# Kernel optimization log

Hardware: AMD Instinct MI355X
Metric: run time of the kernel (lower is better)

Reference implementation:

```python
import jax, jax.numpy as jnp
import numpy as np

# dims
T, B, IN, OUT = 100, 128, 512, 512
# LIF constants (match torch defaults / init_kwargs)
TAU_TRACE, TAU_MEM, TAU_SYN, DT = 20.0, 20.0, 5.0, 1.0
THRESH, SSB = 1.0, 0.03


def setup_inputs() -> dict:
    key = jax.random.key(0)
    k1, k2 = jax.random.split(key)
    input_spikes = (jax.random.uniform(k1, (T, B, IN)) < 0.1).astype(jnp.float32)
    W = jax.random.normal(k2, (OUT, IN), dtype=jnp.float32) * (1.0 / IN ** 0.5)
    return {"input_spikes": input_spikes, "W": W}


def reference(input_spikes, W):
    alpha = jnp.exp(jnp.asarray(-DT / TAU_SYN, jnp.float32))   # synaptic decay
    beta = jnp.exp(jnp.asarray(-DT / TAU_MEM, jnp.float32))    # membrane decay
    gamma = jnp.exp(jnp.asarray(-DT / TAU_TRACE, jnp.float32)) # trace decay
    Tn, Bn, _ = input_spikes.shape
    out_f, in_f = W.shape
    I0 = jnp.zeros((Bn, out_f), jnp.float32)
    U0 = jnp.zeros((Bn, out_f), jnp.float32)
    tr0 = jnp.zeros((Bn, out_f, in_f), jnp.float32)

    def step(carry, x_t):
        I, U, trace = carry
        I = alpha * I + x_t @ W.T                      # (B, out)
        U = beta * U + I
        S = (U >= THRESH).astype(jnp.float32)
        U_pre = U                                      # first U_hist append (pre-reset)
        U = U - S * THRESH                             # reset
        du = jnp.abs(U - THRESH)
        sigma_prime = 1.0 / (1.0 + SSB * du) ** 2      # SuperSpike surrogate
        # eligibility trace: outer product of surrogate grad and input spikes
        trace = gamma * trace + sigma_prime[:, :, None] * x_t[:, None, :]
        U_post = U                                     # second U_hist append (post-reset)
        U = U - S * THRESH                             # second subtraction (as in source)
        return (I, U, trace), (S, U_pre, U_post)

    (_, _, trace), (S, U_pre, U_post) = jax.lax.scan(step, (I0, U0, tr0), input_spikes)
    # interleave pre/post membrane snapshots -> (2T, B, out), matching the torch stack order
    U_hist = jnp.stack([U_pre, U_post], axis=1).reshape(2 * Tn, Bn, out_f)
    return S, U_hist, trace
```

## Files before the change

kernel.cpp:

```cpp
#include <hip/hip_runtime.h>

#define T_STEPS 100
#define B_N     128
#define IN_F    512
#define OUT_F   512
#define KPAD    128

#define ALPHA_D 0.8187307530779818
#define BETA_D  0.9512294245007140

typedef __attribute__((ext_vector_type(8))) short bf16x8;
typedef __attribute__((ext_vector_type(4))) float f32x4;

static __device__ __forceinline__ unsigned int f2bf(float f) {
    union { float f; unsigned int u; } v; v.f = f;
    return (v.u + 0x7FFFu + ((v.u >> 16) & 1u)) >> 16;
}

__global__ __launch_bounds__(256) void transposeW(const float* __restrict__ W,
                                                  float* __restrict__ Wt) {
    __shared__ float tile[32][33];
    const int bx = blockIdx.x & 15;
    const int by = blockIdx.x >> 4;
    const int tx = threadIdx.x & 31;
    const int ty = threadIdx.x >> 5;
#pragma unroll
    for (int k = 0; k < 32; k += 8) {
        int o = by * 32 + ty + k;
        tile[ty + k][tx] = W[o * IN_F + bx * 32 + tx];
    }
    __syncthreads();
#pragma unroll
    for (int k = 0; k < 32; k += 8) {
        int i = bx * 32 + ty + k;
        Wt[i * OUT_F + by * 32 + tx] = tile[tx][ty + k];
    }
}

__global__ __launch_bounds__(256) void syn_plus(const float* __restrict__ x,
                                                const float* __restrict__ Wt,
                                                double* __restrict__ C,
                                                unsigned short* __restrict__ Xbf,
                                                int nconv) {
    const int tid = threadIdx.x;

    if ((int)blockIdx.x < nconv) {
        const int cb = blockIdx.x;
        const int b  = cb & (B_N - 1);
        const int i0 = (cb >> 7) * 128;
#pragma unroll
        for (int r = 0; r < 8; ++r) {
            const int g = tid + r * 256;
            const int i = i0 + (g & 127);
            const int c = g >> 7;
            unsigned int h[4];
#pragma unroll
            for (int jj = 0; jj < 4; ++jj) {
                const int t0 = c * 8 + jj * 2, t1 = t0 + 1;
                float v0 = 0.f, v1 = 0.f;
                if (t0 < T_STEPS) v0 = x[(size_t)t0 * (B_N * IN_F) + b * IN_F + i];
                if (t1 < T_STEPS) v1 = x[(size_t)t1 * (B_N * IN_F) + b * IN_F + i];
                h[jj] = f2bf(v0) | (f2bf(v1) << 16);
            }
            *(uint4*)((char*)Xbf + (size_t)(b * IN_F + i) * (KPAD * 2) + c * 16) =
                make_uint4(h[0], h[1], h[2], h[3]);
        }
        return;
    }

    const int tb = (int)blockIdx.x - nconv;

    __shared__ int s_idx[IN_F];
    __shared__ int s_cnt;

    if (tid < 64) {
        const float* xr = x + (size_t)tb * IN_F;
        int base = 0;
#pragma unroll
        for (int j = 0; j < 8; ++j) {
            const float v = xr[j * 64 + tid];
            const unsigned long long m = __ballot(v > 0.5f);
            if (v > 0.5f) {
                const int pos = base + __popcll(m & ((1ull << tid) - 1ull));
                s_idx[pos] = j * 64 + tid;
            }
            base += __popcll(m);
        }
        if (tid == 0) s_cnt = base;
    }
    __syncthreads();

    const int cnt = s_cnt;
    double c0 = 0.0, c1 = 0.0;
    const float* W0 = Wt + tid;
    const float* W1 = Wt + tid + 256;
    for (int k = 0; k < cnt; ++k) {
        const int i = s_idx[k];
        c0 += (double)W0[(size_t)i * OUT_F];
        c1 += (double)W1[(size_t)i * OUT_F];
    }

    double* Cr = C + (size_t)tb * OUT_F;
    Cr[tid]       = c0;
    Cr[tid + 256] = c1;
}

#define LIF_STEP(BUF, J, CB)                                                   \
    {                                                                          \
        const int t = (CB) * 10 + (J);                                         \
        I = ALPHA_D * I + BUF[J];                                              \
        U = BETA_D * U + I;                                                    \
        const double Sv = (U >= 1.0) ? 1.0 : 0.0;                              \
        S_out[(size_t)t * N + pos] = (float)Sv;                                \
        Uh[(size_t)(2 * t) * N + pos] = (float)U;                              \
        U -= Sv;                                                               \
        Uh[(size_t)(2 * t + 1) * N + pos] = (float)U;                          \
        if (Pq) {                                                              \
            const float du = fabsf((float)U - 1.0f);                           \
            const float dd = 1.0f + 0.03f * du;                                \
            const float pv = __expf(-0.05f * (float)(T_STEPS - 1 - t)) / (dd * dd); \
            const unsigned int hw = f2bf(pv);                                  \
            if ((J) & 1) Pq[(size_t)pos * 64 + (t >> 1)] = plo | (hw << 16);   \
            else plo = hw;                                                     \
        }                                                                      \
        U -= Sv;                                                               \
    }

__global__ __launch_bounds__(256) void lif_pointwise(const double* __restrict__ C,
                                                     float* __restrict__ S_out,
                                                     float* __restrict__ Uh,
                                                     unsigned int* __restrict__ Pq) {
    const int pos = blockIdx.x * 256 + threadIdx.x;
    const size_t N = (size_t)B_N * OUT_F;

    double I = 0.0, U = 0.0;
    double bufA[10], bufB[10];
    unsigned int plo = 0;

#pragma unroll
    for (int j = 0; j < 10; ++j) bufA[j] = C[(size_t)j * N + pos];

    for (int cb = 0; cb < 10; cb += 2) {
#pragma unroll
        for (int j = 0; j < 10; ++j) bufB[j] = C[((size_t)(cb + 1) * 10 + j) * N + pos];
#pragma unroll
        for (int j = 0; j < 10; ++j) LIF_STEP(bufA, j, cb)
        if (cb + 2 < 10) {
#pragma unroll
            for (int j = 0; j < 10; ++j) bufA[j] = C[((size_t)(cb + 2) * 10 + j) * N + pos];
        }
#pragma unroll
        for (int j = 0; j < 10; ++j) LIF_STEP(bufB, j, cb + 1)
    }

    if (Pq) {
#pragma unroll
        for (int k = 0; k < 14; ++k) Pq[(size_t)pos * 64 + 50 + k] = 0u;
    }
}

__global__ __launch_bounds__(256) void trace_mfma2(const unsigned short* __restrict__ Pbf,
                                                   const unsigned short* __restrict__ Xbf,
                                                   float* __restrict__ trace) {
    __shared__ char smem[49152];
    char* const pbase = smem;
    char* const xbase = smem + 32768;

    const int idx  = blockIdx.x;
    const int xcd  = idx & 7;
    const int slot = idx >> 3;
    const int b    = xcd * 16 + (slot >> 5);
    const int tile = slot & 31;
    const int ot   = tile >> 3;
    const int it   = tile & 7;
    const int tid  = threadIdx.x;

    const char* const Pg = (const char*)Pbf + (size_t)(b * OUT_F + ot * 128) * (KPAD * 2);
    const char* const Xg = (const char*)Xbf + (size_t)(b * IN_F + it * 64) * (KPAD * 2);

#pragma unroll
    for (int r = 0; r < 8; ++r) {
        const int chunk = tid + r * 256;
        const int row   = chunk >> 4;
        const int c     = chunk & 15;
        const unsigned int loff = (unsigned int)(row * 256) +
            ((unsigned int)(c * 16) ^ ((unsigned int)(row & 7) << 4));
        *(uint4*)(pbase + loff) = *(const uint4*)(Pg + (size_t)row * 256 + c * 16);
    }
#pragma unroll
    for (int r = 0; r < 4; ++r) {
        const int chunk = tid + r * 256;
        const int row   = chunk >> 4;
        const int c     = chunk & 15;
        const unsigned int loff = (unsigned int)(row * 256) +
            ((unsigned int)(c * 16) ^ ((unsigned int)(row & 7) << 4));
        *(uint4*)(xbase + loff) = *(const uint4*)(Xg + (size_t)row * 256 + c * 16);
    }
    __syncthreads();

    const int w    = tid >> 6;
    const int l    = tid & 63;
    const int lo16 = l & 15;
    const int g4   = l >> 4;

    f32x4 acc[2][4];
#pragma unroll
    for (int m = 0; m < 2; ++m)
#pragma unroll
        for (int n = 0; n < 4; ++n) acc[m][n] = (f32x4){0.f, 0.f, 0.f, 0.f};

#pragma unroll
    for (int kk = 0; kk < 4; ++kk) {
        bf16x8 af[2], bfr[4];
#pragma unroll
        for (int m = 0; m < 2; ++m) {
            const int row = w * 32 + m * 16 + lo16;
            const unsigned int off = (unsigned int)(row * 256 + kk * 64 + g4 * 16)
                                     ^ ((unsigned int)(row & 7) << 4);
            af[m] = *(const bf16x8*)(pbase + off);
        }
#pragma unroll
        for (int n = 0; n < 4; ++n) {
            const int row = n * 16 + lo16;
            const unsigned int off = (unsigned int)(row * 256 + kk * 64 + g4 * 16)
                                     ^ ((unsigned int)(row & 7) << 4);
            bfr[n] = *(const bf16x8*)(xbase + off);
        }
#pragma unroll
        for (int m = 0; m < 2; ++m)
#pragma unroll
            for (int n = 0; n < 4; ++n)
                acc[m][n] = __builtin_amdgcn_mfma_f32_16x16x32_bf16(af[m], bfr[n], acc[m][n], 0, 0, 0);
    }

    __syncthreads();
    float* const obuf = (float*)smem;
#pragma unroll
    for (int m = 0; m < 2; ++m)
#pragma unroll
        for (int n = 0; n < 4; ++n)
#pragma unroll
            for (int rr = 0; rr < 4; ++rr)
                obuf[(w * 32 + m * 16 + g4 * 4 + rr) * 68 + n * 16 + lo16] = acc[m][n][rr];
    __syncthreads();

    float* const tb = trace + (size_t)b * (OUT_F * IN_F) + (size_t)(ot * 128) * IN_F + it * 64;
#pragma unroll
    for (int p = 0; p < 8; ++p) {
        const int row  = p * 16 + (tid >> 4);
        const int col4 = (tid & 15) * 4;
        const f32x4 v = *(const f32x4*)&obuf[row * 68 + col4];
        __builtin_nontemporal_store(v, (f32x4*)(tb + (size_t)row * IN_F + col4));
    }
}

__global__ __launch_bounds__(256) void trace_mfma(const float* __restrict__ x,
                                                  const float* __restrict__ Uh,
                                                  float* __restrict__ trace) {
    __shared__ unsigned short Pa[128 * 128];
    __shared__ unsigned short Xb[128 * 128];

    const int idx  = blockIdx.x;
    const int xcd  = idx & 7;
    const int slot = idx >> 3;
    const int b    = xcd * 16 + (slot >> 4);
    const int tile = slot & 15;
    const int ot   = tile >> 2;
    const int it   = tile & 3;
    const int tid  = threadIdx.x;

    char* const pbase = (char*)Pa;
    char* const xbase = (char*)Xb;

#pragma unroll
    for (int r = 0; r < 8; ++r) {
        const int g  = tid + r * 256;
        const int i  = g & 127;
        const int kg = g >> 7;
        unsigned int h[4];
#pragma unroll
        for (int jj = 0; jj < 4; ++jj) {
            const int t0 = kg * 8 + jj * 2, t1 = t0 + 1;
            float v0 = 0.f, v1 = 0.f;
            if (t0 < T_STEPS) v0 = x[(size_t)t0 * (B_N * IN_F) + b * IN_F + it * 128 + i];
            if (t1 < T_STEPS) v1 = x[(size_t)t1 * (B_N * IN_F) + b * IN_F + it * 128 + i];
            h[jj] = f2bf(v0) | (f2bf(v1) << 16);
        }
        unsigned int off = (unsigned int)(i * 256 + kg * 16) ^ ((unsigned int)(i & 7) << 4);
        *(uint4*)(xbase + off) = make_uint4(h[0], h[1], h[2], h[3]);
    }

#pragma unroll
    for (int r = 0; r < 8; ++r) {
        const int g  = tid + r * 256;
        const int o  = g & 127;
        const int kg = g >> 7;
        unsigned int h[4];
#pragma unroll
        for (int jj = 0; jj < 4; ++jj) {
            unsigned int hw[2];
#pragma unroll
            for (int e = 0; e < 2; ++e) {
                const int t = kg * 8 + jj * 2 + e;
                float p = 0.f;
                if (t < T_STEPS) {
                    const float u  = Uh[(size_t)(2 * t + 1) * (B_N * OUT_F) + b * OUT_F + ot * 128 + o];
                    const float du = fabsf(u - 1.0f);
                    const float d  = 1.0f + 0.03f * du;
                    const float gp = __expf(-0.05f * (float)(T_STEPS - 1 - t));
                    p = gp / (d * d);
                }
                hw[e] = f2bf(p);
            }
            h[jj] = hw[0] | (hw[1] << 16);
        }
        unsigned int off = (unsigned int)(o * 256 + kg * 16) ^ ((unsigned int)(o & 7) << 4);
        *(uint4*)(pbase + off) = make_uint4(h[0], h[1], h[2], h[3]);
    }
    __syncthreads();

    const int w    = tid >> 6;
    const int l    = tid & 63;
    const int wo   = (w >> 1) * 64;
    const int wi   = (w & 1) * 64;
    const int lo16 = l & 15;
    const int g4   = l >> 4;

    f32x4 acc[4][4];
#pragma unroll
    for (int m = 0; m < 4; ++m)
#pragma unroll
        for (int n = 0; n < 4; ++n) acc[m][n] = (f32x4){0.f, 0.f, 0.f, 0.f};

#pragma unroll
    for (int kk = 0; kk < 4; ++kk) {
        bf16x8 af[4], bfr[4];
#pragma unroll
        for (int m = 0; m < 4; ++m) {
            const int row = wo + m * 16 + lo16;
            const unsigned int off = (unsigned int)(row * 256 + kk * 64 + g4 * 16)
                                     ^ ((unsigned int)(row & 7) << 4);
            af[m] = *(const bf16x8*)(pbase + off);
        }
#pragma unroll
        for (int n = 0; n < 4; ++n) {
            const int row = wi + n * 16 + lo16;
            const unsigned int off = (unsigned int)(row * 256 + kk * 64 + g4 * 16)
                                     ^ ((unsigned int)(row & 7) << 4);
            bfr[n] = *(const bf16x8*)(xbase + off);
        }
#pragma unroll
        for (int m = 0; m < 4; ++m)
#pragma unroll
            for (int n = 0; n < 4; ++n)
                acc[m][n] = __builtin_amdgcn_mfma_f32_16x16x32_bf16(af[m], bfr[n], acc[m][n], 0, 0, 0);
    }

    float* tb = trace + (size_t)b * (OUT_F * IN_F);
#pragma unroll
    for (int m = 0; m < 4; ++m) {
#pragma unroll
        for (int rr = 0; rr < 4; ++rr) {
            const int o = ot * 128 + wo + m * 16 + g4 * 4 + rr;
#pragma unroll
            for (int n = 0; n < 4; ++n) {
                const int i = it * 128 + wi + n * 16 + lo16;
                tb[(size_t)o * IN_F + i] = acc[m][n][rr];
            }
        }
    }
}

extern "C" void kernel_launch(void* const* d_in, const int* in_sizes, int n_in,
                              void* d_out, int out_size, void* d_ws, size_t ws_size,
                              hipStream_t stream) {
    const float* x = (const float*)d_in[0];
    const float* W = (const float*)d_in[1];

    float* out   = (float*)d_out;
    float* S_out = out;
    float* Uh    = out + (size_t)T_STEPS * B_N * OUT_F;
    float* trace = Uh + (size_t)2 * T_STEPS * B_N * OUT_F;

    const size_t WT_BYTES = (size_t)IN_F * OUT_F * 4;
    const size_t BF_BYTES = (size_t)B_N * 512 * KPAD * 2;
    const bool   ws_ok    = ws_size >= WT_BYTES + 2 * BF_BYTES;

    float*          Wt  = (float*)d_ws;
    unsigned short* Xbf = (unsigned short*)((char*)d_ws + WT_BYTES);
    unsigned short* Pbf = (unsigned short*)((char*)d_ws + WT_BYTES + BF_BYTES);

    double* C = (double*)trace;

    const int nconv = ws_ok ? 512 : 0;

    transposeW<<<256, 256, 0, stream>>>(W, Wt);
    syn_plus<<<T_STEPS * B_N + nconv, 256, 0, stream>>>(x, Wt, C, Xbf, nconv);
    lif_pointwise<<<B_N * OUT_F / 256, 256, 0, stream>>>(C, S_out, Uh,
                                                         ws_ok ? (unsigned int*)Pbf : nullptr);
    if (ws_ok)
        trace_mfma2<<<32 * B_N, 256, 0, stream>>>(Pbf, Xbf, trace);
    else
        trace_mfma<<<16 * B_N, 256, 0, stream>>>(x, Uh, trace);
}
```

Before: 160.4 us.

## Make trace kernel persistent over input tiles with double-buffered X prefetch

The trace MFMA kernel now launches 512 blocks, each covering one (batch, 128-row output) slab. It keeps the P fragments in registers for the whole slab and loops over the 8 input tiles, prefetching the next X tile into a second LDS buffer while the current one is in use. Output is written straight from the accumulators as scalar nontemporal stores instead of being staged through LDS for 16-byte vector stores. This saves redundant P loads and launch overhead, but the scalar, strided stores may hurt write coalescing on a kernel dominated by the 134 MB trace write, and having fewer blocks lowers parallelism.

Result: slower. 173.3 us (+8.0%).

```diff
diff --git a/kernel.cpp b/kernel.cpp
--- a/kernel.cpp
+++ b/kernel.cpp
@@ -159,24 +159,23 @@
     }
 }
 
-__global__ __launch_bounds__(256) void trace_mfma2(const unsigned short* __restrict__ Pbf,
+__global__ __launch_bounds__(256) void trace_mfma3(const unsigned short* __restrict__ Pbf,
                                                    const unsigned short* __restrict__ Xbf,
                                                    float* __restrict__ trace) {
-    __shared__ char smem[49152];
-    char* const pbase = smem;
-    char* const xbase = smem + 32768;
-
-    const int idx  = blockIdx.x;
-    const int xcd  = idx & 7;
-    const int slot = idx >> 3;
-    const int b    = xcd * 16 + (slot >> 5);
-    const int tile = slot & 31;
-    const int ot   = tile >> 3;
-    const int it   = tile & 7;
-    const int tid  = threadIdx.x;
-
-    const char* const Pg = (const char*)Pbf + (size_t)(b * OUT_F + ot * 128) * (KPAD * 2);
-    const char* const Xg = (const char*)Xbf + (size_t)(b * IN_F + it * 64) * (KPAD * 2);
+    __shared__ char smem[65536];
+    char* const Pl = smem;
+    char* const X0 = smem + 32768;
+    char* const X1 = smem + 49152;
+
+    const int idx = blockIdx.x;
+    const int xcd = idx & 7;
+    const int s   = idx >> 3;
+    const int b   = xcd * 16 + (s >> 2);
+    const int ot  = s & 3;
+    const int tid = threadIdx.x;
+
+    const char* const Pg  = (const char*)Pbf + (size_t)(b * OUT_F + ot * 128) * 256;
+    const char* const Xgb = (const char*)Xbf + (size_t)b * IN_F * 256;
 
 #pragma unroll
     for (int r = 0; r < 8; ++r) {
@@ -185,7 +184,7 @@
         const int c     = chunk & 15;
         const unsigned int loff = (unsigned int)(row * 256) +
             ((unsigned int)(c * 16) ^ ((unsigned int)(row & 7) << 4));
-        *(uint4*)(pbase + loff) = *(const uint4*)(Pg + (size_t)row * 256 + c * 16);
+        *(uint4*)(Pl + loff) = *(const uint4*)(Pg + (size_t)row * 256 + c * 16);
     }
 #pragma unroll
     for (int r = 0; r < 4; ++r) {
@@ -194,7 +193,7 @@
         const int c     = chunk & 15;
         const unsigned int loff = (unsigned int)(row * 256) +
             ((unsigned int)(c * 16) ^ ((unsigned int)(row & 7) << 4));
-        *(uint4*)(xbase + loff) = *(const uint4*)(Xg + (size_t)row * 256 + c * 16);
+        *(uint4*)(X0 + loff) = *(const uint4*)(Xgb + (size_t)row * 256 + c * 16);
     }
     __syncthreads();
 
@@ -203,54 +202,80 @@
     const int lo16 = l & 15;
     const int g4   = l >> 4;
 
-    f32x4 acc[2][4];
-#pragma unroll
-    for (int m = 0; m < 2; ++m)
-#pragma unroll
-        for (int n = 0; n < 4; ++n) acc[m][n] = (f32x4){0.f, 0.f, 0.f, 0.f};
-
-#pragma unroll
-    for (int kk = 0; kk < 4; ++kk) {
-        bf16x8 af[2], bfr[4];
-#pragma unroll
-        for (int m = 0; m < 2; ++m) {
-            const int row = w * 32 + m * 16 + lo16;
+    bf16x8 af[2][4];
+#pragma unroll
+    for (int m = 0; m < 2; ++m) {
+        const int row = w * 32 + m * 16 + lo16;
+#pragma unroll
+        for (int kk = 0; kk < 4; ++kk) {
             const unsigned int off = (unsigned int)(row * 256 + kk * 64 + g4 * 16)
                                      ^ ((unsigned int)(row & 7) << 4);
-            af[m] = *(const bf16x8*)(pbase + off);
-        }
-#pragma unroll
-        for (int n = 0; n < 4; ++n) {
-            const int row = n * 16 + lo16;
-            const unsigned int off = (unsigned int)(row * 256 + kk * 64 + g4 * 16)
-                                     ^ ((unsigned int)(row & 7) << 4);
-            bfr[n] = *(const bf16x8*)(xbase + off);
-        }
+            af[m][kk] = *(const bf16x8*)(Pl + off);
+        }
+    }
+
+    float* const tbase = trace + (size_t)b * (OUT_F * IN_F) + (size_t)(ot * 128) * IN_F;
+
+    for (int it = 0; it < 8; ++it) {
+        char* const Xc = (it & 1) ? X1 : X0;
+        char* const Xn = (it & 1) ? X0 : X1;
+
+        uint4 xr0, xr1, xr2, xr3;
+        int nrow0 = 0, nc0 = 0, nrow1 = 0, nc1 = 0, nrow2 = 0, nc2 = 0, nrow3 = 0, nc3 = 0;
+        if (it < 7) {
+            const char* const Xgn = Xgb + (size_t)(it + 1) * 64 * 256;
+            {   const int chunk = tid;           nrow0 = chunk >> 4; nc0 = chunk & 15;
+                xr0 = *(const uint4*)(Xgn + (size_t)nrow0 * 256 + nc0 * 16); }
+            {   const int chunk = tid + 256;     nrow1 = chunk >> 4; nc1 = chunk & 15;
+                xr1 = *(const uint4*)(Xgn + (size_t)nrow1 * 256 + nc1 * 16); }
+            {   const int chunk = tid + 512;     nrow2 = chunk >> 4; nc2 = chunk & 15;
+                xr2 = *(const uint4*)(Xgn + (size_t)nrow2 * 256 + nc2 * 16); }
+            {   const int chunk = tid + 768;     nrow3 = chunk >> 4; nc3 = chunk & 15;
+                xr3 = *(const uint4*)(Xgn + (size_t)nrow3 * 256 + nc3 * 16); }
+        }
+
+        f32x4 acc[2][4];
 #pragma unroll
         for (int m = 0; m < 2; ++m)
 #pragma unroll
-            for (int n = 0; n < 4; ++n)
-                acc[m][n] = __builtin_amdgcn_mfma_f32_16x16x32_bf16(af[m], bfr[n], acc[m][n], 0, 0, 0);
-    }
-
-    __syncthreads();
-    float* const obuf = (float*)smem;
-#pragma unroll
-    for (int m = 0; m < 2; ++m)
-#pragma unroll
-        for (int n = 0; n < 4; ++n)
-#pragma unroll
-            for (int rr = 0; rr < 4; ++rr)
-                obuf[(w * 32 + m * 16 + g4 * 4 + rr) * 68 + n * 16 + lo16] = acc[m][n][rr];
-    __syncthreads();
-
-    float* const tb = trace + (size_t)b * (OUT_F * IN_F) + (size_t)(ot * 128) * IN_F + it * 64;
-#pragma unroll
-    for (int p = 0; p < 8; ++p) {
-        const int row  = p * 16 + (tid >> 4);
-        const int col4 = (tid & 15) * 4;
-        const f32x4 v = *(const f32x4*)&obuf[row * 68 + col4];
-        __builtin_nontemporal_store(v, (f32x4*)(tb + (size_t)row * IN_F + col4));
+            for (int n = 0; n < 4; ++n) acc[m][n] = (f32x4){0.f, 0.f, 0.f, 0.f};
+
+#pragma unroll
+        for (int kk = 0; kk < 4; ++kk) {
+            bf16x8 bfr[4];
+#pragma unroll
+            for (int n = 0; n < 4; ++n) {
+                const int row = n * 16 + lo16;
+                const unsigned int off = (unsigned int)(row * 256 + kk * 64 + g4 * 16)
+                                         ^ ((unsigned int)(row & 7) << 4);
+                bfr[n] = *(const bf16x8*)(Xc + off);
+            }
+#pragma unroll
+            for (int m = 0; m < 2; ++m)
+#pragma unroll
+                for (int n = 0; n < 4; ++n)
+                    acc[m][n] = __builtin_amdgcn_mfma_f32_16x16x32_bf16(af[m][kk], bfr[n], acc[m][n], 0, 0, 0);
+        }
+
+        if (it < 7) {
+            *(uint4*)(Xn + ((unsigned int)(nrow0 * 256) + ((unsigned int)(nc0 * 16) ^ ((unsigned int)(nrow0 & 7) << 4)))) = xr0;
+            *(uint4*)(Xn + ((unsigned int)(nrow1 * 256) + ((unsigned int)(nc1 * 16) ^ ((unsigned int)(nrow1 & 7) << 4)))) = xr1;
+            *(uint4*)(Xn + ((unsigned int)(nrow2 * 256) + ((unsigned int)(nc2 * 16) ^ ((unsigned int)(nrow2 & 7) << 4)))) = xr2;
+            *(uint4*)(Xn + ((unsigned int)(nrow3 * 256) + ((unsigned int)(nc3 * 16) ^ ((unsigned int)(nrow3 & 7) << 4)))) = xr3;
+        }
+
+#pragma unroll
+        for (int m = 0; m < 2; ++m)
+#pragma unroll
+            for (int rr = 0; rr < 4; ++rr) {
+                const int o = w * 32 + m * 16 + g4 * 4 + rr;
+                float* const orow = tbase + (size_t)o * IN_F + it * 64 + lo16;
+#pragma unroll
+                for (int n = 0; n < 4; ++n)
+                    __builtin_nontemporal_store(acc[m][n][rr], orow + n * 16);
+            }
+
+        if (it < 7) __syncthreads();
     }
 }
 
@@ -399,7 +424,7 @@
     lif_pointwise<<<B_N * OUT_F / 256, 256, 0, stream>>>(C, S_out, Uh,
                                                          ws_ok ? (unsigned int*)Pbf : nullptr);
     if (ws_ok)
-        trace_mfma2<<<32 * B_N, 256, 0, stream>>>(Pbf, Xbf, trace);
+        trace_mfma3<<<512, 256, 0, stream>>>(Pbf, Xbf, trace);
     else
         trace_mfma<<<16 * B_N, 256, 0, stream>>>(x, Uh, trace);
 }
```
